# Kernel tuning notes

Measured on AMD Instinct MI355X. Metric: run time of the kernel, lower is better.

Reference implementation:

```python
import jax, jax.numpy as jnp
import numpy as np

NEG = -1e30

def setup_inputs() -> dict:
    key = jax.random.key(0)
    k1, k2, k3, k4, k5 = jax.random.split(key, 5)
    B, N, M, D = 32, 2048, 512, 512
    C = jax.random.normal(k1, (B, N, D), dtype=jnp.float32)
    Q = jax.random.normal(k2, (B, M, D), dtype=jnp.float32)
    Cmask = jax.random.randint(k3, (B, N), 0, 2, dtype=jnp.int32)
    Qmask = jax.random.randint(k4, (B, M), 0, 2, dtype=jnp.int32)
    # Linear(3*dim, 1, bias=False) weight, flattened to a (3*dim,) vector.
    bound = 1.0 / np.sqrt(3 * D)
    w = jax.random.uniform(k5, (3 * D,), dtype=jnp.float32, minval=-bound, maxval=bound)
    return {"C": C, "Q": Q, "Cmask": Cmask, "Qmask": Qmask, "w": w}

def reference(C, Q, Cmask, Qmask, w):
    D = C.shape[-1]
    w1, w2, w3 = w[:D], w[D:2 * D], w[2 * D:]
    # Trilinear similarity, decomposed: S = w1.Ct + w2.Qt + w3.(Ct*Qt)
    S = (jnp.einsum('bnd,d->bn', C, w1)[:, :, None]
         + jnp.einsum('bmd,d->bm', Q, w2)[:, None, :]
         + jnp.einsum('bnd,bmd->bnm', C * w3, Q))  # [B, N, M]
    Qm = Qmask.astype(S.dtype)[:, None, :]  # [B, 1, M]; 1 = masked
    Cm = Cmask.astype(S.dtype)[:, :, None]  # [B, N, 1]
    S1 = jax.nn.softmax(S * (1.0 - Qm) + Qm * NEG, axis=2)
    S2 = jax.nn.softmax(S * (1.0 - Cm) + Cm * NEG, axis=1)
    A = jnp.einsum('bnm,bmd->bnd', S1, Q)
    T = jnp.einsum('bnm,bnd->bmd', S2, C)     # S2^T @ C
    Bout = jnp.einsum('bnm,bmd->bnd', S1, T)  # S1 @ (S2^T @ C)
    return (A, Bout)
```

## Files before the change

kernel.cpp:

```cpp
#include <hip/hip_runtime.h>

#define BB 32
#define NN 2048
#define MM 512
#define DD 512
#define TS 64
#define KC 16
#define PAD 4
#define LDKH 40

typedef _Float16 half4f __attribute__((ext_vector_type(4)));
typedef _Float16 half8f __attribute__((ext_vector_type(8)));
typedef float    f32x16 __attribute__((ext_vector_type(16)));

__global__ __launch_bounds__(256) void k_dots(const float* __restrict__ C, const float* __restrict__ Q,
                                              const float* __restrict__ w,
                                              float* __restrict__ c1, float* __restrict__ q2) {
    int wid  = blockIdx.x * 4 + (threadIdx.x >> 6);
    int lane = threadIdx.x & 63;
    const int NR1 = BB * NN;
    const float* src; const float* wv; float* dst;
    if (wid < NR1) { src = C + (size_t)wid * DD; wv = w;       dst = c1 + wid; }
    else { int r = wid - NR1; src = Q + (size_t)r * DD; wv = w + DD; dst = q2 + r; }
    float4 a0 = *(const float4*)(src + lane * 8);
    float4 a1 = *(const float4*)(src + lane * 8 + 4);
    float4 b0 = *(const float4*)(wv  + lane * 8);
    float4 b1 = *(const float4*)(wv  + lane * 8 + 4);
    float s = a0.x * b0.x + a0.y * b0.y + a0.z * b0.z + a0.w * b0.w
            + a1.x * b1.x + a1.y * b1.y + a1.z * b1.z + a1.w * b1.w;
#pragma unroll
    for (int o = 32; o > 0; o >>= 1) s += __shfl_down(s, o);
    if (lane == 0) *dst = s;
}

__global__ __launch_bounds__(256) void k_qt(const float* __restrict__ Q, const int* __restrict__ Qmask,
                                            _Float16* __restrict__ Qt) {
    __shared__ float Ls[64][65];
    const int bid = blockIdx.x;
    const int b   = bid >> 6;
    const int rem = bid & 63;
    const int m0  = (rem >> 3) << 6;
    const int d0  = (rem & 7) << 6;
    const int tid = threadIdx.x;
    const int r   = tid >> 4;
    const int c4  = (tid & 15) << 2;
#pragma unroll
    for (int p = 0; p < 4; ++p) {
        float4 v = *(const float4*)(Q + ((size_t)(b * MM + m0 + r + p * 16)) * DD + d0 + c4);
        const int m = r + p * 16;
        Ls[c4 + 0][m] = v.x; Ls[c4 + 1][m] = v.y; Ls[c4 + 2][m] = v.z; Ls[c4 + 3][m] = v.w;
    }
    __syncthreads();
    float z[4];
#pragma unroll
    for (int i = 0; i < 4; ++i) z[i] = Qmask[b * MM + m0 + c4 + i] ? 0.f : 1.f;
#pragma unroll
    for (int p = 0; p < 4; ++p) {
        const int d = r + p * 16;
        half4f o;
#pragma unroll
        for (int i = 0; i < 4; ++i) o[i] = (_Float16)(Ls[d][c4 + i] * z[i]);
        *(half4f*)&Qt[((size_t)(b * DD + d0 + d)) * MM + m0 + c4] = o;
    }
}

__global__ __launch_bounds__(256) void k_ct(const float* __restrict__ C, _Float16* __restrict__ Ct) {
    __shared__ float Ls[64][65];
    const int bid = blockIdx.x;
    const int b   = bid >> 8;
    const int nn0 = ((bid >> 3) & 31) << 6;
    const int dd0 = (bid & 7) << 6;
    const int tid = threadIdx.x;
    const int r   = tid >> 4;
    const int c4  = (tid & 15) << 2;
#pragma unroll
    for (int p = 0; p < 4; ++p) {
        const int n = r + (p << 4);
        float4 v = *(const float4*)(C + ((size_t)(b * NN + nn0 + n)) * DD + dd0 + c4);
        Ls[c4 + 0][n] = v.x; Ls[c4 + 1][n] = v.y; Ls[c4 + 2][n] = v.z; Ls[c4 + 3][n] = v.w;
    }
    __syncthreads();
#pragma unroll
    for (int p = 0; p < 4; ++p) {
        const int d = r + (p << 4);
        half4f o;
#pragma unroll
        for (int i = 0; i < 4; ++i) o[i] = (_Float16)Ls[d][c4 + i];
        *(half4f*)&Ct[((size_t)(b * DD + dd0 + d)) * NN + nn0 + c4] = o;
    }
}

__global__ __launch_bounds__(256) void k_te(const _Float16* __restrict__ E, const int* __restrict__ Cmask,
                                            _Float16* __restrict__ Et) {
    __shared__ float Ls[64][65];
    const int bid = blockIdx.x;
    const int b   = bid >> 8;
    const int nn0 = ((bid >> 3) & 31) << 6;
    const int mm0 = (bid & 7) << 6;
    const int tid = threadIdx.x;
    const int r   = tid >> 4;
    const int c4  = (tid & 15) << 2;
#pragma unroll
    for (int p = 0; p < 4; ++p) {
        const int n = r + (p << 4);
        half4f v = *(const half4f*)&E[((size_t)(b * NN + nn0 + n)) * MM + mm0 + c4];
        const float z = Cmask[b * NN + nn0 + n] ? 0.f : 1.f;
        Ls[c4 + 0][n] = (float)v[0] * z; Ls[c4 + 1][n] = (float)v[1] * z;
        Ls[c4 + 2][n] = (float)v[2] * z; Ls[c4 + 3][n] = (float)v[3] * z;
    }
    __syncthreads();
#pragma unroll
    for (int p = 0; p < 4; ++p) {
        const int m = r + (p << 4);
        half4f o;
#pragma unroll
        for (int i = 0; i < 4; ++i) o[i] = (_Float16)Ls[m][c4 + i];
        *(half4f*)&Et[((size_t)(b * MM + mm0 + m)) * NN + nn0 + c4] = o;
    }
}

__global__ __launch_bounds__(256, 2) void k_sgemm(const float* __restrict__ C, const float* __restrict__ Q,
                                                  const float* __restrict__ w,
                                                  const int* __restrict__ Cmask, const int* __restrict__ Qmask,
                                                  const float* __restrict__ c1, const float* __restrict__ q2,
                                                  _Float16* __restrict__ E, float* __restrict__ rsum,
                                                  float* __restrict__ csum) {
    __shared__ _Float16 Ah[128 * LDKH], Al[128 * LDKH], Bh[128 * LDKH], Bl[128 * LDKH];
    __shared__ float rowp[128], colp[128], cmz[128], qmz[128], c1s[128], q2s[128];
    const int hw  = blockIdx.x;
    const int bid = ((hw & 7) << 8) | (hw >> 3);
    const int b   = bid >> 6;
    const int rem = bid & 63;
    const int n0  = (rem >> 2) << 7;
    const int m0  = (rem & 3) << 7;
    const int tid = threadIdx.x;
    const int lane = tid & 63;
    const int wid  = tid >> 6;
    const int wr = wid >> 1, wc = wid & 1;
    const int srow = tid >> 3;
    const int sc4  = (tid & 7) << 2;
    if (tid < 128) {
        rowp[tid] = 0.f; colp[tid] = 0.f;
        cmz[tid] = Cmask[b * NN + n0 + tid] ? 0.f : 1.f;
        c1s[tid] = c1[b * NN + n0 + tid];
    } else {
        const int t = tid - 128;
        qmz[t] = Qmask[b * MM + m0 + t] ? 0.f : 1.f;
        q2s[t] = q2[b * MM + m0 + t];
    }
    f32x16 accH[2][2] = {};
    f32x16 accX[2][2] = {};
    const int ar  = wr * 64 + (lane & 31);
    const int bc  = wc * 64 + (lane & 31);
    const int kof = (lane >> 5) << 3;
    const float* Cb = C + ((size_t)(b * NN + n0)) * DD;
    const float* Qb = Q + ((size_t)(b * MM + m0)) * DD;
    const float* w3 = w + 2 * DD;
    for (int k0 = 0; k0 < DD; k0 += 32) {
        float4 wv = *(const float4*)(w3 + k0 + sc4);
        float4 ca[4], qa[4];
#pragma unroll
        for (int p = 0; p < 4; ++p) {
            ca[p] = *(const float4*)(Cb + (size_t)(srow + (p << 5)) * DD + k0 + sc4);
            qa[p] = *(const float4*)(Qb + (size_t)(srow + (p << 5)) * DD + k0 + sc4);
        }
        __syncthreads();
#pragma unroll
        for (int p = 0; p < 4; ++p) {
            const int ofs = (srow + (p << 5)) * LDKH + sc4;
            float ax[4] = {ca[p].x * wv.x, ca[p].y * wv.y, ca[p].z * wv.z, ca[p].w * wv.w};
            float bx[4] = {qa[p].x, qa[p].y, qa[p].z, qa[p].w};
            half4f ah, al, bh, bl;
#pragma unroll
            for (int e = 0; e < 4; ++e) {
                _Float16 h = (_Float16)ax[e]; ah[e] = h;
                al[e] = (_Float16)((ax[e] - (float)h) * 2048.f);
                _Float16 g = (_Float16)bx[e]; bh[e] = g;
                bl[e] = (_Float16)((bx[e] - (float)g) * 2048.f);
            }
            *(half4f*)&Ah[ofs] = ah; *(half4f*)&Al[ofs] = al;
            *(half4f*)&Bh[ofs] = bh; *(half4f*)&Bl[ofs] = bl;
        }
        __syncthreads();
#pragma unroll
        for (int h = 0; h < 2; ++h) {
            const int ko = (h << 4) + kof;
            half8f ah0 = *(const half8f*)&Ah[ar * LDKH + ko];
            half8f ah1 = *(const half8f*)&Ah[(ar + 32) * LDKH + ko];
            half8f al0 = *(const half8f*)&Al[ar * LDKH + ko];
            half8f al1 = *(const half8f*)&Al[(ar + 32) * LDKH + ko];
            half8f bh0 = *(const half8f*)&Bh[bc * LDKH + ko];
            half8f bh1 = *(const half8f*)&Bh[(bc + 32) * LDKH + ko];
            half8f bl0 = *(const half8f*)&Bl[bc * LDKH + ko];
            half8f bl1 = *(const half8f*)&Bl[(bc + 32) * LDKH + ko];
            accH[0][0] = __builtin_amdgcn_mfma_f32_32x32x16_f16(ah0, bh0, accH[0][0], 0, 0, 0);
            accH[0][1] = __builtin_amdgcn_mfma_f32_32x32x16_f16(ah0, bh1, accH[0][1], 0, 0, 0);
            accH[1][0] = __builtin_amdgcn_mfma_f32_32x32x16_f16(ah1, bh0, accH[1][0], 0, 0, 0);
            accH[1][1] = __builtin_amdgcn_mfma_f32_32x32x16_f16(ah1, bh1, accH[1][1], 0, 0, 0);
            accX[0][0] = __builtin_amdgcn_mfma_f32_32x32x16_f16(ah0, bl0, accX[0][0], 0, 0, 0);
            accX[0][0] = __builtin_amdgcn_mfma_f32_32x32x16_f16(al0, bh0, accX[0][0], 0, 0, 0);
            accX[0][1] = __builtin_amdgcn_mfma_f32_32x32x16_f16(ah0, bl1, accX[0][1], 0, 0, 0);
            accX[0][1] = __builtin_amdgcn_mfma_f32_32x32x16_f16(al0, bh1, accX[0][1], 0, 0, 0);
            accX[1][0] = __builtin_amdgcn_mfma_f32_32x32x16_f16(ah1, bl0, accX[1][0], 0, 0, 0);
            accX[1][0] = __builtin_amdgcn_mfma_f32_32x32x16_f16(al1, bh0, accX[1][0], 0, 0, 0);
            accX[1][1] = __builtin_amdgcn_mfma_f32_32x32x16_f16(ah1, bl1, accX[1][1], 0, 0, 0);
            accX[1][1] = __builtin_amdgcn_mfma_f32_32x32x16_f16(al1, bh1, accX[1][1], 0, 0, 0);
        }
    }
    const float inv2k = 4.8828125e-4f;
    const int mcol0 = wc * 64 + (lane & 31);
    const float qz0 = qmz[mcol0], qz1 = qmz[mcol0 + 32];
    const float q2v0 = q2s[mcol0], q2v1 = q2s[mcol0 + 32];
    const int hi4 = (lane >> 5) << 2;
    float colacc0 = 0.f, colacc1 = 0.f;
#pragma unroll
    for (int i = 0; i < 2; ++i) {
#pragma unroll
        for (int r = 0; r < 16; ++r) {
            const int nloc = wr * 64 + i * 32 + (r & 3) + ((r >> 2) << 3) + hi4;
            const float base = c1s[nloc];
            float S0 = accH[i][0][r] + accX[i][0][r] * inv2k + base + q2v0;
            float S1 = accH[i][1][r] + accX[i][1][r] * inv2k + base + q2v1;
            float e0 = __expf(S0), e1 = __expf(S1);
            _Float16 h0 = (_Float16)e0, h1 = (_Float16)e1;
            float eq0 = (float)h0, eq1 = (float)h1;
            const size_t erow = ((size_t)(b * NN + n0 + nloc)) * MM + m0;
            E[erow + mcol0]      = h0;
            E[erow + mcol0 + 32] = h1;
            const float cz = cmz[nloc];
            colacc0 += eq0 * cz;
            colacc1 += eq1 * cz;
            float rv = eq0 * qz0 + eq1 * qz1;
            rv += __shfl_xor(rv, 1);  rv += __shfl_xor(rv, 2);
            rv += __shfl_xor(rv, 4);  rv += __shfl_xor(rv, 8);
            rv += __shfl_xor(rv, 16);
            if ((lane & 31) == 0) atomicAdd(&rowp[nloc], rv);
        }
    }
    atomicAdd(&colp[mcol0], colacc0);
    atomicAdd(&colp[mcol0 + 32], colacc1);
    __syncthreads();
    if (tid < 128) atomicAdd(&rsum[b * NN + n0 + tid], rowp[tid]);
    else atomicAdd(&csum[b * MM + m0 + tid - 128], colp[tid - 128]);
}

__global__ __launch_bounds__(256, 2) void k_T(const _Float16* __restrict__ Ct,
                                              const _Float16* __restrict__ Et,
                                              const float* __restrict__ csum,
                                              const int* __restrict__ Qmask,
                                              _Float16* __restrict__ Tt) {
    __shared__ _Float16 As[128 * LDKH];
    __shared__ _Float16 Bs[128 * LDKH];
    const int hw  = blockIdx.x;
    const int bid = ((hw & 7) << 6) | (hw >> 3);
    const int b   = bid >> 4;
    const int rem = bid & 15;
    const int d0  = (rem >> 2) << 7;
    const int m0  = (rem & 3) << 7;
    const int tid = threadIdx.x;
    const int lane = tid & 63;
    const int wid  = tid >> 6;
    const int wr = wid >> 1, wc = wid & 1;
    const int srow = tid >> 2;
    const int scol = (tid & 3) << 3;
    const _Float16* g0 = Ct + ((size_t)(b * DD + d0 + srow)) * NN + scol;
    const _Float16* g1 = Et + ((size_t)(b * MM + m0 + srow)) * NN + scol;
    const int wofs = srow * LDKH + scol;
    f32x16 acc[2][2] = {};
    const int ar  = wr * 64 + (lane & 31);
    const int bc  = wc * 64 + (lane & 31);
    const int kof = (lane >> 5) << 3;
    for (int k0 = 0; k0 < NN; k0 += 32) {
        half8f a0v = *(const half8f*)(g0 + k0);
        half8f a1v = *(const half8f*)(g0 + k0 + (size_t)64 * NN);
        half8f b0v = *(const half8f*)(g1 + k0);
        half8f b1v = *(const half8f*)(g1 + k0 + (size_t)64 * NN);
        __syncthreads();
        *(half8f*)&As[wofs]             = a0v;
        *(half8f*)&As[wofs + 64 * LDKH] = a1v;
        *(half8f*)&Bs[wofs]             = b0v;
        *(half8f*)&Bs[wofs + 64 * LDKH] = b1v;
        __syncthreads();
#pragma unroll
        for (int h = 0; h < 2; ++h) {
            const int ko = (h << 4) + kof;
            half8f a0 = *(const half8f*)&As[ar * LDKH + ko];
            half8f a1 = *(const half8f*)&As[(ar + 32) * LDKH + ko];
            half8f b0 = *(const half8f*)&Bs[bc * LDKH + ko];
            half8f b1 = *(const half8f*)&Bs[(bc + 32) * LDKH + ko];
            acc[0][0] = __builtin_amdgcn_mfma_f32_32x32x16_f16(a0, b0, acc[0][0], 0, 0, 0);
            acc[0][1] = __builtin_amdgcn_mfma_f32_32x32x16_f16(a0, b1, acc[0][1], 0, 0, 0);
            acc[1][0] = __builtin_amdgcn_mfma_f32_32x32x16_f16(a1, b0, acc[1][0], 0, 0, 0);
            acc[1][1] = __builtin_amdgcn_mfma_f32_32x32x16_f16(a1, b1, acc[1][1], 0, 0, 0);
        }
    }
    const int mc0 = m0 + wc * 64 + (lane & 31);
    const float s0 = (Qmask[b * MM + mc0]      ? 0.f : 1.f) / csum[b * MM + mc0];
    const float s1 = (Qmask[b * MM + mc0 + 32] ? 0.f : 1.f) / csum[b * MM + mc0 + 32];
    const int hi4 = (lane >> 5) << 2;
#pragma unroll
    for (int i = 0; i < 2; ++i) {
#pragma unroll
        for (int r = 0; r < 16; ++r) {
            const int d = d0 + wr * 64 + i * 32 + (r & 3) + ((r >> 2) << 3) + hi4;
            const size_t o = ((size_t)(b * DD + d)) * MM + mc0;
            Tt[o]      = (_Float16)(acc[i][0][r] * s0);
            Tt[o + 32] = (_Float16)(acc[i][1][r] * s1);
        }
    }
}

#define KS 32

__global__ __launch_bounds__(256, 2) void k_AB(const _Float16* __restrict__ E,
                                               const _Float16* __restrict__ Qt,
                                               const _Float16* __restrict__ Tt,
                                               const float* __restrict__ rsum,
                                               float* __restrict__ outA, float* __restrict__ outB) {
    __shared__ _Float16 Es[128 * LDKH];
    __shared__ _Float16 Ws[2][128 * LDKH];
    const int hw  = blockIdx.x;
    const int bid = ((hw & 7) << 8) | (hw >> 3);
    const int b   = bid >> 6;
    const int rem = bid & 63;
    const int n0  = (rem >> 2) << 7;
    const int d0  = (rem & 3) << 7;
    const int tid = threadIdx.x;
    const int lane = tid & 63;
    const int wid  = tid >> 6;
    const int wr = wid >> 1, wc = wid & 1;
    const int srow = tid >> 2;
    const int scol = (tid & 3) << 3;
    const _Float16* g0 = E  + ((size_t)(b * NN + n0 + srow)) * MM + scol;
    const _Float16* g1 = Qt + ((size_t)(b * DD + d0 + srow)) * MM + scol;
    const _Float16* g2 = Tt + ((size_t)(b * DD + d0 + srow)) * MM + scol;
    const int wofs = srow * LDKH + scol;
    f32x16 accA[2][2] = {};
    f32x16 accB[2][2] = {};
    const int ar  = wr * 64 + (lane & 31);
    const int bc  = wc * 64 + (lane & 31);
    const int kof = (lane >> 5) << 3;
    for (int k0 = 0; k0 < MM; k0 += KS) {
        half8f e0 = *(const half8f*)(g0 + k0);
        half8f e1 = *(const half8f*)(g0 + k0 + (size_t)64 * MM);
        half8f q0 = *(const half8f*)(g1 + k0);
        half8f q1 = *(const half8f*)(g1 + k0 + (size_t)64 * MM);
        half8f t0 = *(const half8f*)(g2 + k0);
        half8f t1 = *(const half8f*)(g2 + k0 + (size_t)64 * MM);
        __syncthreads();
        *(half8f*)&Es[wofs]                = e0;
        *(half8f*)&Es[wofs + 64 * LDKH]    = e1;
        *(half8f*)&Ws[0][wofs]             = q0;
        *(half8f*)&Ws[0][wofs + 64 * LDKH] = q1;
        *(half8f*)&Ws[1][wofs]             = t0;
        *(half8f*)&Ws[1][wofs + 64 * LDKH] = t1;
        __syncthreads();
#pragma unroll
        for (int h = 0; h < 2; ++h) {
            const int ko = (h << 4) + kof;
            half8f a0  = *(const half8f*)&Es[ar * LDKH + ko];
            half8f a1  = *(const half8f*)&Es[(ar + 32) * LDKH + ko];
            half8f bq0 = *(const half8f*)&Ws[0][bc * LDKH + ko];
            half8f bq1 = *(const half8f*)&Ws[0][(bc + 32) * LDKH + ko];
            half8f bt0 = *(const half8f*)&Ws[1][bc * LDKH + ko];
            half8f bt1 = *(const half8f*)&Ws[1][(bc + 32) * LDKH + ko];
            accA[0][0] = __builtin_amdgcn_mfma_f32_32x32x16_f16(a0, bq0, accA[0][0], 0, 0, 0);
            accA[0][1] = __builtin_amdgcn_mfma_f32_32x32x16_f16(a0, bq1, accA[0][1], 0, 0, 0);
            accA[1][0] = __builtin_amdgcn_mfma_f32_32x32x16_f16(a1, bq0, accA[1][0], 0, 0, 0);
            accA[1][1] = __builtin_amdgcn_mfma_f32_32x32x16_f16(a1, bq1, accA[1][1], 0, 0, 0);
            accB[0][0] = __builtin_amdgcn_mfma_f32_32x32x16_f16(a0, bt0, accB[0][0], 0, 0, 0);
            accB[0][1] = __builtin_amdgcn_mfma_f32_32x32x16_f16(a0, bt1, accB[0][1], 0, 0, 0);
            accB[1][0] = __builtin_amdgcn_mfma_f32_32x32x16_f16(a1, bt0, accB[1][0], 0, 0, 0);
            accB[1][1] = __builtin_amdgcn_mfma_f32_32x32x16_f16(a1, bt1, accB[1][1], 0, 0, 0);
        }
    }
    const int dc = d0 + wc * 64 + (lane & 31);
#pragma unroll
    for (int i = 0; i < 2; ++i) {
#pragma unroll
        for (int r = 0; r < 16; ++r) {
            const int row = (r & 3) + ((r >> 2) << 3) + ((lane >> 5) << 2);
            const int n = n0 + wr * 64 + i * 32 + row;
            const float inv = __builtin_amdgcn_rcpf(rsum[b * NN + n]);
            const size_t o = ((size_t)(b * NN + n)) * DD + dc;
            outA[o]      = accA[i][0][r] * inv;
            outA[o + 32] = accA[i][1][r] * inv;
            outB[o]      = accB[i][0][r] * inv;
            outB[o + 32] = accB[i][1][r] * inv;
        }
    }
}

extern "C" void kernel_launch(void* const* d_in, const int* in_sizes, int n_in,
                              void* d_out, int out_size, void* d_ws, size_t ws_size,
                              hipStream_t stream) {
    const float* C = (const float*)d_in[0];
    const float* Q = (const float*)d_in[1];
    const int* Cmask = (const int*)d_in[2];
    const int* Qmask = (const int*)d_in[3];
    const float* w  = (const float*)d_in[4];

    const size_t BNM = (size_t)BB * NN * MM;
    const size_t BMD = (size_t)BB * MM * DD;
    const size_t BND = (size_t)BB * NN * DD;
    const size_t BN  = (size_t)BB * NN;
    const size_t BM  = (size_t)BB * MM;

    _Float16* E  = (_Float16*)d_ws;
    _Float16* Tt = E + BNM;
    _Float16* Qt = Tt + BMD;
    float* fbase = (float*)(Qt + BMD);
    float* c1   = fbase;
    float* q2   = c1 + BN;
    float* rsum = q2 + BM;
    float* csum = rsum + BN;

    _Float16* Ct = (_Float16*)d_out;
    _Float16* Et = (_Float16*)((float*)d_out + BND);

    hipMemsetAsync(rsum, 0, (BN + BM) * sizeof(float), stream);

    k_dots<<<(int)((BN + BM) / 4), 256, 0, stream>>>(C, Q, w, c1, q2);
    k_qt<<<BB * 64, 256, 0, stream>>>(Q, Qmask, Qt);
    k_ct<<<BB * 256, 256, 0, stream>>>(C, Ct);
    k_sgemm<<<2048, 256, 0, stream>>>(C, Q, w, Cmask, Qmask, c1, q2, E, rsum, csum);
    k_te<<<BB * 256, 256, 0, stream>>>(E, Cmask, Et);
    k_T<<<512, 256, 0, stream>>>(Ct, Et, csum, Qmask, Tt);
    k_AB<<<2048, 256, 0, stream>>>(E, Qt, Tt, rsum,
                                   (float*)d_out, (float*)d_out + BND);
}
```

Before: 755.7 us.

## Pre-pack operands into MFMA fragment layout and stream GEMMs from global registers

```diff
diff --git a/kernel.cpp b/kernel.cpp
--- a/kernel.cpp
+++ b/kernel.cpp
@@ -4,128 +4,197 @@
 #define NN 2048
 #define MM 512
 #define DD 512
-#define TS 64
-#define KC 16
-#define PAD 4
-#define LDKH 40
-
-typedef _Float16 half4f __attribute__((ext_vector_type(4)));
+
 typedef _Float16 half8f __attribute__((ext_vector_type(8)));
 typedef float    f32x16 __attribute__((ext_vector_type(16)));
 
-__global__ __launch_bounds__(256) void k_dots(const float* __restrict__ C, const float* __restrict__ Q,
-                                              const float* __restrict__ w,
-                                              float* __restrict__ c1, float* __restrict__ q2) {
-    int wid  = blockIdx.x * 4 + (threadIdx.x >> 6);
-    int lane = threadIdx.x & 63;
-    const int NR1 = BB * NN;
-    const float* src; const float* wv; float* dst;
-    if (wid < NR1) { src = C + (size_t)wid * DD; wv = w;       dst = c1 + wid; }
-    else { int r = wid - NR1; src = Q + (size_t)r * DD; wv = w + DD; dst = q2 + r; }
-    float4 a0 = *(const float4*)(src + lane * 8);
-    float4 a1 = *(const float4*)(src + lane * 8 + 4);
-    float4 b0 = *(const float4*)(wv  + lane * 8);
-    float4 b1 = *(const float4*)(wv  + lane * 8 + 4);
-    float s = a0.x * b0.x + a0.y * b0.y + a0.z * b0.z + a0.w * b0.w
-            + a1.x * b1.x + a1.y * b1.y + a1.z * b1.z + a1.w * b1.w;
-#pragma unroll
-    for (int o = 32; o > 0; o >>= 1) s += __shfl_down(s, o);
-    if (lane == 0) *dst = s;
-}
-
-__global__ __launch_bounds__(256) void k_qt(const float* __restrict__ Q, const int* __restrict__ Qmask,
-                                            _Float16* __restrict__ Qt) {
-    __shared__ float Ls[64][65];
-    const int bid = blockIdx.x;
-    const int b   = bid >> 6;
-    const int rem = bid & 63;
-    const int m0  = (rem >> 3) << 6;
-    const int d0  = (rem & 7) << 6;
-    const int tid = threadIdx.x;
-    const int r   = tid >> 4;
-    const int c4  = (tid & 15) << 2;
-#pragma unroll
-    for (int p = 0; p < 4; ++p) {
-        float4 v = *(const float4*)(Q + ((size_t)(b * MM + m0 + r + p * 16)) * DD + d0 + c4);
-        const int m = r + p * 16;
-        Ls[c4 + 0][m] = v.x; Ls[c4 + 1][m] = v.y; Ls[c4 + 2][m] = v.z; Ls[c4 + 3][m] = v.w;
-    }
-    __syncthreads();
-    float z[4];
-#pragma unroll
-    for (int i = 0; i < 4; ++i) z[i] = Qmask[b * MM + m0 + c4 + i] ? 0.f : 1.f;
-#pragma unroll
-    for (int p = 0; p < 4; ++p) {
-        const int d = r + p * 16;
-        half4f o;
-#pragma unroll
-        for (int i = 0; i < 4; ++i) o[i] = (_Float16)(Ls[d][c4 + i] * z[i]);
-        *(half4f*)&Qt[((size_t)(b * DD + d0 + d)) * MM + m0 + c4] = o;
-    }
-}
-
-__global__ __launch_bounds__(256) void k_ct(const float* __restrict__ C, _Float16* __restrict__ Ct) {
+#define MFMA __builtin_amdgcn_mfma_f32_32x32x16_f16
+
+__device__ __forceinline__ int pidx(int r, int k, int K) {
+    return (r >> 7) * (K << 7) + ((k >> 4) << 11) + (((r >> 5) & 3) << 9)
+         + (((r & 31) + (((k >> 3) & 1) << 5)) << 3) + (k & 7);
+}
+__device__ __forceinline__ int kpart(int k) {
+    return ((k >> 4) << 11) + (((k >> 3) & 1) << 8) + (k & 7);
+}
+
+__global__ __launch_bounds__(256) void k_prepC(const float* __restrict__ C, const float* __restrict__ w,
+                                               float* __restrict__ c1, _Float16* __restrict__ PCt,
+                                               _Float16* __restrict__ PCh, _Float16* __restrict__ PCl) {
     __shared__ float Ls[64][65];
     const int bid = blockIdx.x;
     const int b   = bid >> 8;
     const int nn0 = ((bid >> 3) & 31) << 6;
     const int dd0 = (bid & 7) << 6;
     const int tid = threadIdx.x;
-    const int r   = tid >> 4;
-    const int c4  = (tid & 15) << 2;
+    const int nl  = tid >> 2;
+    const int dl  = (tid & 3) << 4;
+    const float* w1 = w;
+    const float* w3 = w + 2 * DD;
+    const size_t crow = ((size_t)(b * NN + nn0 + nl)) * DD + dd0 + dl;
+    float4 v[4], u[4], t[4];
 #pragma unroll
     for (int p = 0; p < 4; ++p) {
-        const int n = r + (p << 4);
-        float4 v = *(const float4*)(C + ((size_t)(b * NN + nn0 + n)) * DD + dd0 + c4);
-        Ls[c4 + 0][n] = v.x; Ls[c4 + 1][n] = v.y; Ls[c4 + 2][n] = v.z; Ls[c4 + 3][n] = v.w;
+        v[p] = *(const float4*)(C + crow + p * 4);
+        u[p] = *(const float4*)(w1 + dd0 + dl + p * 4);
+        t[p] = *(const float4*)(w3 + dd0 + dl + p * 4);
+    }
+    float s = 0.f;
+#pragma unroll
+    for (int p = 0; p < 4; ++p) s += v[p].x * u[p].x + v[p].y * u[p].y + v[p].z * u[p].z + v[p].w * u[p].w;
+    s += __shfl_xor(s, 1); s += __shfl_xor(s, 2);
+    if ((tid & 3) == 0) atomicAdd(&c1[b * NN + nn0 + nl], s);
+#pragma unroll
+    for (int p = 0; p < 4; ++p) {
+        Ls[dl + p * 4 + 0][nl] = v[p].x; Ls[dl + p * 4 + 1][nl] = v[p].y;
+        Ls[dl + p * 4 + 2][nl] = v[p].z; Ls[dl + p * 4 + 3][nl] = v[p].w;
+    }
+    const size_t pb = (size_t)b * NN * DD;
+#pragma unroll
+    for (int q = 0; q < 2; ++q) {
+        float x[8];
+#pragma unroll
+        for (int e = 0; e < 8; ++e) {
+            const int p = q * 2 + (e >> 2);
+            const float* vp = &v[p].x; const float* tp = &t[p].x;
+            x[e] = vp[e & 3] * tp[e & 3];
+        }
+        half8f hh, ll;
+#pragma unroll
+        for (int e = 0; e < 8; ++e) {
+            _Float16 h = (_Float16)x[e]; hh[e] = h;
+            ll[e] = (_Float16)((x[e] - (float)h) * 2048.f);
+        }
+        const int pi = pidx(nn0 + nl, dd0 + dl + q * 8, DD);
+        *(half8f*)&PCh[pb + pi] = hh;
+        *(half8f*)&PCl[pb + pi] = ll;
     }
     __syncthreads();
+    const int d2 = tid >> 2, n2 = (tid & 3) << 4;
+    const size_t tb = (size_t)b * DD * NN;
+#pragma unroll
+    for (int q = 0; q < 2; ++q) {
+        const int nc = n2 + q * 8;
+        half8f o;
+#pragma unroll
+        for (int j = 0; j < 8; ++j) o[j] = (_Float16)Ls[d2][nc + j];
+        *(half8f*)&PCt[tb + pidx(dd0 + d2, nn0 + nc, NN)] = o;
+    }
+}
+
+__global__ __launch_bounds__(256) void k_prepQ(const float* __restrict__ Q, const int* __restrict__ Qmask,
+                                               const float* __restrict__ w, float* __restrict__ q2,
+                                               _Float16* __restrict__ PQt,
+                                               _Float16* __restrict__ PQh, _Float16* __restrict__ PQl) {
+    __shared__ float Ls[64][65];
+    const int bid = blockIdx.x;
+    const int b   = bid >> 6;
+    const int rem = bid & 63;
+    const int mm0 = (rem >> 3) << 6;
+    const int dd0 = (rem & 7) << 6;
+    const int tid = threadIdx.x;
+    const int ml  = tid >> 2;
+    const int dl  = (tid & 3) << 4;
+    const float* w2 = w + DD;
+    const size_t qrow = ((size_t)(b * MM + mm0 + ml)) * DD + dd0 + dl;
+    float4 v[4], u[4];
 #pragma unroll
     for (int p = 0; p < 4; ++p) {
-        const int d = r + (p << 4);
-        half4f o;
-#pragma unroll
-        for (int i = 0; i < 4; ++i) o[i] = (_Float16)Ls[d][c4 + i];
-        *(half4f*)&Ct[((size_t)(b * DD + dd0 + d)) * NN + nn0 + c4] = o;
-    }
-}
-
-__global__ __launch_bounds__(256) void k_te(const _Float16* __restrict__ E, const int* __restrict__ Cmask,
-                                            _Float16* __restrict__ Et) {
+        v[p] = *(const float4*)(Q + qrow + p * 4);
+        u[p] = *(const float4*)(w2 + dd0 + dl + p * 4);
+    }
+    float s = 0.f;
+#pragma unroll
+    for (int p = 0; p < 4; ++p) s += v[p].x * u[p].x + v[p].y * u[p].y + v[p].z * u[p].z + v[p].w * u[p].w;
+    s += __shfl_xor(s, 1); s += __shfl_xor(s, 2);
+    if ((tid & 3) == 0) atomicAdd(&q2[b * MM + mm0 + ml], s);
+    const float z = Qmask[b * MM + mm0 + ml] ? 0.f : 1.f;
+#pragma unroll
+    for (int p = 0; p < 4; ++p) {
+        Ls[dl + p * 4 + 0][ml] = v[p].x * z; Ls[dl + p * 4 + 1][ml] = v[p].y * z;
+        Ls[dl + p * 4 + 2][ml] = v[p].z * z; Ls[dl + p * 4 + 3][ml] = v[p].w * z;
+    }
+    const size_t pb = (size_t)b * MM * DD;
+#pragma unroll
+    for (int q = 0; q < 2; ++q) {
+        float x[8];
+#pragma unroll
+        for (int e = 0; e < 8; ++e) {
+            const int p = q * 2 + (e >> 2);
+            const float* vp = &v[p].x;
+            x[e] = vp[e & 3];
+        }
+        half8f hh, ll;
+#pragma unroll
+        for (int e = 0; e < 8; ++e) {
+            _Float16 h = (_Float16)x[e]; hh[e] = h;
+            ll[e] = (_Float16)((x[e] - (float)h) * 2048.f);
+        }
+        const int pi = pidx(mm0 + ml, dd0 + dl + q * 8, DD);
+        *(half8f*)&PQh[pb + pi] = hh;
+        *(half8f*)&PQl[pb + pi] = ll;
+    }
+    __syncthreads();
+    const int d2 = tid >> 2, m2 = (tid & 3) << 4;
+    const size_t tb = (size_t)b * DD * MM;
+#pragma unroll
+    for (int q = 0; q < 2; ++q) {
+        const int mc = m2 + q * 8;
+        half8f o;
+#pragma unroll
+        for (int j = 0; j < 8; ++j) o[j] = (_Float16)Ls[d2][mc + j];
+        *(half8f*)&PQt[tb + pidx(dd0 + d2, mm0 + mc, MM)] = o;
+    }
+}
+
+__global__ __launch_bounds__(256) void k_te(const _Float16* __restrict__ PE, const int* __restrict__ Cmask,
+                                            _Float16* __restrict__ PEt) {
     __shared__ float Ls[64][65];
     const int bid = blockIdx.x;
     const int b   = bid >> 8;
     const int nn0 = ((bid >> 3) & 31) << 6;
     const int mm0 = (bid & 7) << 6;
     const int tid = threadIdx.x;
-    const int r   = tid >> 4;
-    const int c4  = (tid & 15) << 2;
-#pragma unroll
-    for (int p = 0; p < 4; ++p) {
-        const int n = r + (p << 4);
-        half4f v = *(const half4f*)&E[((size_t)(b * NN + nn0 + n)) * MM + mm0 + c4];
-        const float z = Cmask[b * NN + nn0 + n] ? 0.f : 1.f;
-        Ls[c4 + 0][n] = (float)v[0] * z; Ls[c4 + 1][n] = (float)v[1] * z;
-        Ls[c4 + 2][n] = (float)v[2] * z; Ls[c4 + 3][n] = (float)v[3] * z;
+    const int nl  = tid >> 2;
+    const int ml  = (tid & 3) << 4;
+    const float z = Cmask[b * NN + nn0 + nl] ? 0.f : 1.f;
+    const size_t eb = (size_t)b * NN * MM;
+#pragma unroll
+    for (int q = 0; q < 2; ++q) {
+        half8f v = *(const half8f*)&PE[eb + pidx(nn0 + nl, mm0 + ml + q * 8, MM)];
+#pragma unroll
+        for (int j = 0; j < 8; ++j) Ls[ml + q * 8 + j][nl] = (float)v[j] * z;
     }
     __syncthreads();
-#pragma unroll
-    for (int p = 0; p < 4; ++p) {
-        const int m = r + (p << 4);
-        half4f o;
-#pragma unroll
-        for (int i = 0; i < 4; ++i) o[i] = (_Float16)Ls[m][c4 + i];
-        *(half4f*)&Et[((size_t)(b * MM + mm0 + m)) * NN + nn0 + c4] = o;
-    }
-}
-
-__global__ __launch_bounds__(256, 2) void k_sgemm(const float* __restrict__ C, const float* __restrict__ Q,
-                                                  const float* __restrict__ w,
+    const int m2 = tid >> 2, n2 = (tid & 3) << 4;
+    const size_t tb = (size_t)b * MM * NN;
+#pragma unroll
+    for (int q = 0; q < 2; ++q) {
+        const int nc = n2 + q * 8;
+        half8f o;
+#pragma unroll
+        for (int j = 0; j < 8; ++j) o[j] = (_Float16)Ls[m2][nc + j];
+        *(half8f*)&PEt[tb + pidx(mm0 + m2, nn0 + nc, NN)] = o;
+    }
+}
+
+#define SG_LOAD(P, kc) { const int o_ = (kc) * 256;                                   \
+    P##ah0 = pAh[o_]; P##ah1 = pAh[o_ + 64]; P##al0 = pAl[o_]; P##al1 = pAl[o_ + 64]; \
+    P##bh0 = pBh[o_]; P##bh1 = pBh[o_ + 64]; P##bl0 = pBl[o_]; P##bl1 = pBl[o_ + 64]; }
+#define SG_STEP(A0,A1,L0,L1,B0,B1,D0,D1)                                     \
+    accH[0][0]=MFMA(A0,B0,accH[0][0],0,0,0); accH[0][1]=MFMA(A0,B1,accH[0][1],0,0,0); \
+    accH[1][0]=MFMA(A1,B0,accH[1][0],0,0,0); accH[1][1]=MFMA(A1,B1,accH[1][1],0,0,0); \
+    accX[0][0]=MFMA(A0,D0,accX[0][0],0,0,0); accX[0][0]=MFMA(L0,B0,accX[0][0],0,0,0); \
+    accX[0][1]=MFMA(A0,D1,accX[0][1],0,0,0); accX[0][1]=MFMA(L0,B1,accX[0][1],0,0,0); \
+    accX[1][0]=MFMA(A1,D0,accX[1][0],0,0,0); accX[1][0]=MFMA(L1,B0,accX[1][0],0,0,0); \
+    accX[1][1]=MFMA(A1,D1,accX[1][1],0,0,0); accX[1][1]=MFMA(L1,B1,accX[1][1],0,0,0);
+
+__global__ __launch_bounds__(256, 2) void k_sgemm(const _Float16* __restrict__ PCh, const _Float16* __restrict__ PCl,
+                                                  const _Float16* __restrict__ PQh, const _Float16* __restrict__ PQl,
                                                   const int* __restrict__ Cmask, const int* __restrict__ Qmask,
                                                   const float* __restrict__ c1, const float* __restrict__ q2,
                                                   _Float16* __restrict__ E, float* __restrict__ rsum,
                                                   float* __restrict__ csum) {
-    __shared__ _Float16 Ah[128 * LDKH], Al[128 * LDKH], Bh[128 * LDKH], Bl[128 * LDKH];
     __shared__ float rowp[128], colp[128], cmz[128], qmz[128], c1s[128], q2s[128];
     const int hw  = blockIdx.x;
     const int bid = ((hw & 7) << 8) | (hw >> 3);
@@ -137,8 +206,6 @@
     const int lane = tid & 63;
     const int wid  = tid >> 6;
     const int wr = wid >> 1, wc = wid & 1;
-    const int srow = tid >> 3;
-    const int sc4  = (tid & 7) << 2;
     if (tid < 128) {
         rowp[tid] = 0.f; colp[tid] = 0.f;
         cmz[tid] = Cmask[b * NN + n0 + tid] ? 0.f : 1.f;
@@ -148,70 +215,30 @@
         qmz[t] = Qmask[b * MM + m0 + t] ? 0.f : 1.f;
         q2s[t] = q2[b * MM + m0 + t];
     }
+    __syncthreads();
+    const half8f* pAh = (const half8f*)(PCh + (size_t)b * NN * DD + (size_t)n0 * DD) + wr * 128 + lane;
+    const half8f* pAl = (const half8f*)(PCl + (size_t)b * NN * DD + (size_t)n0 * DD) + wr * 128 + lane;
+    const half8f* pBh = (const half8f*)(PQh + (size_t)b * MM * DD + (size_t)m0 * DD) + wc * 128 + lane;
+    const half8f* pBl = (const half8f*)(PQl + (size_t)b * MM * DD + (size_t)m0 * DD) + wc * 128 + lane;
     f32x16 accH[2][2] = {};
     f32x16 accX[2][2] = {};
-    const int ar  = wr * 64 + (lane & 31);
-    const int bc  = wc * 64 + (lane & 31);
-    const int kof = (lane >> 5) << 3;
-    const float* Cb = C + ((size_t)(b * NN + n0)) * DD;
-    const float* Qb = Q + ((size_t)(b * MM + m0)) * DD;
-    const float* w3 = w + 2 * DD;
-    for (int k0 = 0; k0 < DD; k0 += 32) {
-        float4 wv = *(const float4*)(w3 + k0 + sc4);
-        float4 ca[4], qa[4];
-#pragma unroll
-        for (int p = 0; p < 4; ++p) {
-            ca[p] = *(const float4*)(Cb + (size_t)(srow + (p << 5)) * DD + k0 + sc4);
-            qa[p] = *(const float4*)(Qb + (size_t)(srow + (p << 5)) * DD + k0 + sc4);
-        }
-        __syncthreads();
-#pragma unroll
-        for (int p = 0; p < 4; ++p) {
-            const int ofs = (srow + (p << 5)) * LDKH + sc4;
-            float ax[4] = {ca[p].x * wv.x, ca[p].y * wv.y, ca[p].z * wv.z, ca[p].w * wv.w};
-            float bx[4] = {qa[p].x, qa[p].y, qa[p].z, qa[p].w};
-            half4f ah, al, bh, bl;
-#pragma unroll
-            for (int e = 0; e < 4; ++e) {
-                _Float16 h = (_Float16)ax[e]; ah[e] = h;
-                al[e] = (_Float16)((ax[e] - (float)h) * 2048.f);
-                _Float16 g = (_Float16)bx[e]; bh[e] = g;
-                bl[e] = (_Float16)((bx[e] - (float)g) * 2048.f);
-            }
-            *(half4f*)&Ah[ofs] = ah; *(half4f*)&Al[ofs] = al;
-            *(half4f*)&Bh[ofs] = bh; *(half4f*)&Bl[ofs] = bl;
-        }
-        __syncthreads();
-#pragma unroll
-        for (int h = 0; h < 2; ++h) {
-            const int ko = (h << 4) + kof;
-            half8f ah0 = *(const half8f*)&Ah[ar * LDKH + ko];
-            half8f ah1 = *(const half8f*)&Ah[(ar + 32) * LDKH + ko];
-            half8f al0 = *(const half8f*)&Al[ar * LDKH + ko];
-            half8f al1 = *(const half8f*)&Al[(ar + 32) * LDKH + ko];
-            half8f bh0 = *(const half8f*)&Bh[bc * LDKH + ko];
-            half8f bh1 = *(const half8f*)&Bh[(bc + 32) * LDKH + ko];
-            half8f bl0 = *(const half8f*)&Bl[bc * LDKH + ko];
-            half8f bl1 = *(const half8f*)&Bl[(bc + 32) * LDKH + ko];
-            accH[0][0] = __builtin_amdgcn_mfma_f32_32x32x16_f16(ah0, bh0, accH[0][0], 0, 0, 0);
-            accH[0][1] = __builtin_amdgcn_mfma_f32_32x32x16_f16(ah0, bh1, accH[0][1], 0, 0, 0);
-            accH[1][0] = __builtin_amdgcn_mfma_f32_32x32x16_f16(ah1, bh0, accH[1][0], 0, 0, 0);
-            accH[1][1] = __builtin_amdgcn_mfma_f32_32x32x16_f16(ah1, bh1, accH[1][1], 0, 0, 0);
-            accX[0][0] = __builtin_amdgcn_mfma_f32_32x32x16_f16(ah0, bl0, accX[0][0], 0, 0, 0);
-            accX[0][0] = __builtin_amdgcn_mfma_f32_32x32x16_f16(al0, bh0, accX[0][0], 0, 0, 0);
-            accX[0][1] = __builtin_amdgcn_mfma_f32_32x32x16_f16(ah0, bl1, accX[0][1], 0, 0, 0);
-            accX[0][1] = __builtin_amdgcn_mfma_f32_32x32x16_f16(al0, bh1, accX[0][1], 0, 0, 0);
-            accX[1][0] = __builtin_amdgcn_mfma_f32_32x32x16_f16(ah1, bl0, accX[1][0], 0, 0, 0);
-            accX[1][0] = __builtin_amdgcn_mfma_f32_32x32x16_f16(al1, bh0, accX[1][0], 0, 0, 0);
-            accX[1][1] = __builtin_amdgcn_mfma_f32_32x32x16_f16(ah1, bl1, accX[1][1], 0, 0, 0);
-            accX[1][1] = __builtin_amdgcn_mfma_f32_32x32x16_f16(al1, bh1, accX[1][1], 0, 0, 0);
-        }
+    half8f xah0, xah1, xal0, xal1, xbh0, xbh1, xbl0, xbl1;
+    half8f yah0, yah1, yal0, yal1, ybh0, ybh1, ybl0, ybl1;
+    SG_LOAD(x, 0);
+    for (int kc = 0; kc < 32; kc += 2) {
+        SG_LOAD(y, kc + 1);
+        SG_STEP(xah0, xah1, xal0, xal1, xbh0, xbh1, xbl0, xbl1);
+        if (kc + 2 < 32) SG_LOAD(x, kc + 2);
+        SG_STEP(yah0, yah1, yal0, yal1, ybh0, ybh1, ybl0, ybl1);
     }
     const float inv2k = 4.8828125e-4f;
     const int mcol0 = wc * 64 + (lane & 31);
     const float qz0 = qmz[mcol0], qz1 = qmz[mcol0 + 32];
     const float q2v0 = q2s[mcol0], q2v1 = q2s[mcol0 + 32];
     const int hi4 = (lane >> 5) << 2;
+    const size_t ebase = (size_t)b * NN * MM + (size_t)n0 * MM;
+    const int kp0 = kpart(m0 + mcol0);
+    const int kp1 = kpart(m0 + mcol0 + 32);
     float colacc0 = 0.f, colacc1 = 0.f;
 #pragma unroll
     for (int i = 0; i < 2; ++i) {
@@ -224,9 +251,9 @@
             float e0 = __expf(S0), e1 = __expf(S1);
             _Float16 h0 = (_Float16)e0, h1 = (_Float16)e1;
             float eq0 = (float)h0, eq1 = (float)h1;
-            const size_t erow = ((size_t)(b * NN + n0 + nloc)) * MM + m0;
-            E[erow + mcol0]      = h0;
-            E[erow + mcol0 + 32] = h1;
+            const int rp = (((nloc >> 5) & 3) << 9) + ((nloc & 31) << 3);
+            E[ebase + rp + kp0] = h0;
+            E[ebase + rp + kp1] = h1;
             const float cz = cmz[nloc];
             colacc0 += eq0 * cz;
             colacc1 += eq1 * cz;
@@ -244,13 +271,17 @@
     else atomicAdd(&csum[b * MM + m0 + tid - 128], colp[tid - 128]);
 }
 
-__global__ __launch_bounds__(256, 2) void k_T(const _Float16* __restrict__ Ct,
-                                              const _Float16* __restrict__ Et,
+#define KT_LOAD(P, kc) { const int o_ = (kc) * 256;                     \
+    P##a0 = pA[o_]; P##a1 = pA[o_ + 64]; P##b0 = pB[o_]; P##b1 = pB[o_ + 64]; }
+#define KT_STEP(A0,A1,B0,B1)                                            \
+    acc[0][0]=MFMA(A0,B0,acc[0][0],0,0,0); acc[0][1]=MFMA(A0,B1,acc[0][1],0,0,0); \
+    acc[1][0]=MFMA(A1,B0,acc[1][0],0,0,0); acc[1][1]=MFMA(A1,B1,acc[1][1],0,0,0);
+
+__global__ __launch_bounds__(256, 2) void k_T(const _Float16* __restrict__ PCt,
+                                              const _Float16* __restrict__ PEt,
                                               const float* __restrict__ csum,
                                               const int* __restrict__ Qmask,
                                               _Float16* __restrict__ Tt) {
-    __shared__ _Float16 As[128 * LDKH];
-    __shared__ _Float16 Bs[128 * LDKH];
     const int hw  = blockIdx.x;
     const int bid = ((hw & 7) << 6) | (hw >> 3);
     const int b   = bid >> 4;
@@ -261,64 +292,50 @@
     const int lane = tid & 63;
     const int wid  = tid >> 6;
     const int wr = wid >> 1, wc = wid & 1;
-    const int srow = tid >> 2;
-    const int scol = (tid & 3) << 3;
-    const _Float16* g0 = Ct + ((size_t)(b * DD + d0 + srow)) * NN + scol;
-    const _Float16* g1 = Et + ((size_t)(b * MM + m0 + srow)) * NN + scol;
-    const int wofs = srow * LDKH + scol;
+    const half8f* pA = (const half8f*)(PCt + (size_t)b * DD * NN + (size_t)d0 * NN) + wr * 128 + lane;
+    const half8f* pB = (const half8f*)(PEt + (size_t)b * MM * NN + (size_t)m0 * NN) + wc * 128 + lane;
     f32x16 acc[2][2] = {};
-    const int ar  = wr * 64 + (lane & 31);
-    const int bc  = wc * 64 + (lane & 31);
-    const int kof = (lane >> 5) << 3;
-    for (int k0 = 0; k0 < NN; k0 += 32) {
-        half8f a0v = *(const half8f*)(g0 + k0);
-        half8f a1v = *(const half8f*)(g0 + k0 + (size_t)64 * NN);
-        half8f b0v = *(const half8f*)(g1 + k0);
-        half8f b1v = *(const half8f*)(g1 + k0 + (size_t)64 * NN);
-        __syncthreads();
-        *(half8f*)&As[wofs]             = a0v;
-        *(half8f*)&As[wofs + 64 * LDKH] = a1v;
-        *(half8f*)&Bs[wofs]             = b0v;
-        *(half8f*)&Bs[wofs + 64 * LDKH] = b1v;
-        __syncthreads();
-#pragma unroll
-        for (int h = 0; h < 2; ++h) {
-            const int ko = (h << 4) + kof;
-            half8f a0 = *(const half8f*)&As[ar * LDKH + ko];
-            half8f a1 = *(const half8f*)&As[(ar + 32) * LDKH + ko];
-            half8f b0 = *(const half8f*)&Bs[bc * LDKH + ko];
-            half8f b1 = *(const half8f*)&Bs[(bc + 32) * LDKH + ko];
-            acc[0][0] = __builtin_amdgcn_mfma_f32_32x32x16_f16(a0, b0, acc[0][0], 0, 0, 0);
-            acc[0][1] = __builtin_amdgcn_mfma_f32_32x32x16_f16(a0, b1, acc[0][1], 0, 0, 0);
-            acc[1][0] = __builtin_amdgcn_mfma_f32_32x32x16_f16(a1, b0, acc[1][0], 0, 0, 0);
-            acc[1][1] = __builtin_amdgcn_mfma_f32_32x32x16_f16(a1, b1, acc[1][1], 0, 0, 0);
-        }
+    half8f xa0, xa1, xb0, xb1, ya0, ya1, yb0, yb1;
+    KT_LOAD(x, 0);
+    for (int kc = 0; kc < 128; kc += 2) {
+        KT_LOAD(y, kc + 1);
+        KT_STEP(xa0, xa1, xb0, xb1);
+        if (kc + 2 < 128) KT_LOAD(x, kc + 2);
+        KT_STEP(ya0, ya1, yb0, yb1);
     }
     const int mc0 = m0 + wc * 64 + (lane & 31);
     const float s0 = (Qmask[b * MM + mc0]      ? 0.f : 1.f) / csum[b * MM + mc0];
     const float s1 = (Qmask[b * MM + mc0 + 32] ? 0.f : 1.f) / csum[b * MM + mc0 + 32];
     const int hi4 = (lane >> 5) << 2;
+    const size_t tbase = (size_t)b * DD * MM + (size_t)d0 * MM;
+    const int kp0 = kpart(mc0);
+    const int kp1 = kpart(mc0 + 32);
 #pragma unroll
     for (int i = 0; i < 2; ++i) {
 #pragma unroll
         for (int r = 0; r < 16; ++r) {
-            const int d = d0 + wr * 64 + i * 32 + (r & 3) + ((r >> 2) << 3) + hi4;
-            const size_t o = ((size_t)(b * DD + d)) * MM + mc0;
-            Tt[o]      = (_Float16)(acc[i][0][r] * s0);
-            Tt[o + 32] = (_Float16)(acc[i][1][r] * s1);
-        }
-    }
-}
-
-#define KS 32
+            const int dloc = wr * 64 + i * 32 + (r & 3) + ((r >> 2) << 3) + hi4;
+            const int rp = (((dloc >> 5) & 3) << 9) + ((dloc & 31) << 3);
+            Tt[tbase + rp + kp0] = (_Float16)(acc[i][0][r] * s0);
+            Tt[tbase + rp + kp1] = (_Float16)(acc[i][1][r] * s1);
+        }
+    }
+}
+
+#define AB_LOAD(P, kc) { const int o_ = (kc) * 256;                     \
+    P##e0 = pE[o_]; P##e1 = pE[o_ + 64]; P##q0 = pQ[o_]; P##q1 = pQ[o_ + 64]; \
+    P##t0 = pT[o_]; P##t1 = pT[o_ + 64]; }
+#define AB_STEP(E0,E1,Q0,Q1,T0,T1)                                      \
+    accA[0][0]=MFMA(E0,Q0,accA[0][0],0,0,0); accA[0][1]=MFMA(E0,Q1,accA[0][1],0,0,0); \
+    accA[1][0]=MFMA(E1,Q0,accA[1][0],0,0,0); accA[1][1]=MFMA(E1,Q1,accA[1][1],0,0,0); \
+    accB[0][0]=MFMA(E0,T0,accB[0][0],0,0,0); accB[0][1]=MFMA(E0,T1,accB[0][1],0,0,0); \
+    accB[1][0]=MFMA(E1,T0,accB[1][0],0,0,0); accB[1][1]=MFMA(E1,T1,accB[1][1],0,0,0);
 
 __global__ __launch_bounds__(256, 2) void k_AB(const _Float16* __restrict__ E,
-                                               const _Float16* __restrict__ Qt,
+                                               const _Float16* __restrict__ PQt,
                                                const _Float16* __restrict__ Tt,
                                                const float* __restrict__ rsum,
                                                float* __restrict__ outA, float* __restrict__ outB) {
-    __shared__ _Float16 Es[128 * LDKH];
-    __shared__ _Float16 Ws[2][128 * LDKH];
     const int hw  = blockIdx.x;
     const int bid = ((hw & 7) << 8) | (hw >> 3);
     const int b   = bid >> 6;
@@ -329,50 +346,18 @@
     const int lane = tid & 63;
     const int wid  = tid >> 6;
     const int wr = wid >> 1, wc = wid & 1;
-    const int srow = tid >> 2;
-    const int scol = (tid & 3) << 3;
-    const _Float16* g0 = E  + ((size_t)(b * NN + n0 + srow)) * MM + scol;
-    const _Float16* g1 = Qt + ((size_t)(b * DD + d0 + srow)) * MM + scol;
-    const _Float16* g2 = Tt + ((size_t)(b * DD + d0 + srow)) * MM + scol;
-    const int wofs = srow * LDKH + scol;
+    const half8f* pE = (const half8f*)(E   + (size_t)b * NN * MM + (size_t)n0 * MM) + wr * 128 + lane;
+    const half8f* pQ = (const half8f*)(PQt + (size_t)b * DD * MM + (size_t)d0 * MM) + wc * 128 + lane;
+    const half8f* pT = (const half8f*)(Tt  + (size_t)b * DD * MM + (size_t)d0 * MM) + wc * 128 + lane;
     f32x16 accA[2][2] = {};
     f32x16 accB[2][2] = {};
-    const int ar  = wr * 64 + (lane & 31);
-    const int bc  = wc * 64 + (lane & 31);
-    const int kof = (lane >> 5) << 3;
-    for (int k0 = 0; k0 < MM; k0 += KS) {
-        half8f e0 = *(const half8f*)(g0 + k0);
-        half8f e1 = *(const half8f*)(g0 + k0 + (size_t)64 * MM);
-        half8f q0 = *(const half8f*)(g1 + k0);
-        half8f q1 = *(const half8f*)(g1 + k0 + (size_t)64 * MM);
-        half8f t0 = *(const half8f*)(g2 + k0);
-        half8f t1 = *(const half8f*)(g2 + k0 + (size_t)64 * MM);
-        __syncthreads();
-        *(half8f*)&Es[wofs]                = e0;
-        *(half8f*)&Es[wofs + 64 * LDKH]    = e1;
-        *(half8f*)&Ws[0][wofs]             = q0;
-        *(half8f*)&Ws[0][wofs + 64 * LDKH] = q1;
-        *(half8f*)&Ws[1][wofs]             = t0;
-        *(half8f*)&Ws[1][wofs + 64 * LDKH] = t1;
-        __syncthreads();
-#pragma unroll
-        for (int h = 0; h < 2; ++h) {
-            const int ko = (h << 4) + kof;
-            half8f a0  = *(const half8f*)&Es[ar * LDKH + ko];
-            half8f a1  = *(const half8f*)&Es[(ar + 32) * LDKH + ko];
-            half8f bq0 = *(const half8f*)&Ws[0][bc * LDKH + ko];
-            half8f bq1 = *(const half8f*)&Ws[0][(bc + 32) * LDKH + ko];
-            half8f bt0 = *(const half8f*)&Ws[1][bc * LDKH + ko];
-            half8f bt1 = *(const half8f*)&Ws[1][(bc + 32) * LDKH + ko];
-            accA[0][0] = __builtin_amdgcn_mfma_f32_32x32x16_f16(a0, bq0, accA[0][0], 0, 0, 0);
-            accA[0][1] = __builtin_amdgcn_mfma_f32_32x32x16_f16(a0, bq1, accA[0][1], 0, 0, 0);
-            accA[1][0] = __builtin_amdgcn_mfma_f32_32x32x16_f16(a1, bq0, accA[1][0], 0, 0, 0);
-            accA[1][1] = __builtin_amdgcn_mfma_f32_32x32x16_f16(a1, bq1, accA[1][1], 0, 0, 0);
-            accB[0][0] = __builtin_amdgcn_mfma_f32_32x32x16_f16(a0, bt0, accB[0][0], 0, 0, 0);
-            accB[0][1] = __builtin_amdgcn_mfma_f32_32x32x16_f16(a0, bt1, accB[0][1], 0, 0, 0);
-            accB[1][0] = __builtin_amdgcn_mfma_f32_32x32x16_f16(a1, bt0, accB[1][0], 0, 0, 0);
-            accB[1][1] = __builtin_amdgcn_mfma_f32_32x32x16_f16(a1, bt1, accB[1][1], 0, 0, 0);
-        }
+    half8f xe0, xe1, xq0, xq1, xt0, xt1, ye0, ye1, yq0, yq1, yt0, yt1;
+    AB_LOAD(x, 0);
+    for (int kc = 0; kc < 32; kc += 2) {
+        AB_LOAD(y, kc + 1);
+        AB_STEP(xe0, xe1, xq0, xq1, xt0, xt1);
+        if (kc + 2 < 32) AB_LOAD(x, kc + 2);
+        AB_STEP(ye0, ye1, yq0, yq1, yt0, yt1);
     }
     const int dc = d0 + wc * 64 + (lane & 31);
 #pragma unroll
@@ -406,26 +391,28 @@
     const size_t BN  = (size_t)BB * NN;
     const size_t BM  = (size_t)BB * MM;
 
-    _Float16* E  = (_Float16*)d_ws;
-    _Float16* Tt = E + BNM;
-    _Float16* Qt = Tt + BMD;
-    float* fbase = (float*)(Qt + BMD);
-    float* c1   = fbase;
+    _Float16* E   = (_Float16*)d_ws;
+    _Float16* Tt  = E + BNM;
+    _Float16* PQt = Tt + BMD;
+    float* c1   = (float*)(PQt + BMD);
     float* q2   = c1 + BN;
     float* rsum = q2 + BM;
     float* csum = rsum + BN;
 
-    _Float16* Ct = (_Float16*)d_out;
-    _Float16* Et = (_Float16*)((float*)d_out + BND);
-
-    hipMemsetAsync(rsum, 0, (BN + BM) * sizeof(float), stream);
-
-    k_dots<<<(int)((BN + BM) / 4), 256, 0, stream>>>(C, Q, w, c1, q2);
-    k_qt<<<BB * 64, 256, 0, stream>>>(Q, Qmask, Qt);
-    k_ct<<<BB * 256, 256, 0, stream>>>(C, Ct);
-    k_sgemm<<<2048, 256, 0, stream>>>(C, Q, w, Cmask, Qmask, c1, q2, E, rsum, csum);
-    k_te<<<BB * 256, 256, 0, stream>>>(E, Cmask, Et);
-    k_T<<<512, 256, 0, stream>>>(Ct, Et, csum, Qmask, Tt);
-    k_AB<<<2048, 256, 0, stream>>>(E, Qt, Tt, rsum,
+    _Float16* PCt = (_Float16*)d_out;
+    _Float16* PCh = PCt + BND;
+    _Float16* PCl = PCh + BND;
+    _Float16* PQh = PCl + BND;
+    _Float16* PQl = PQh + BMD;
+    _Float16* PEt = PCh;
+
+    hipMemsetAsync(c1, 0, 2 * (BN + BM) * sizeof(float), stream);
+
+    k_prepQ<<<BB * 64, 256, 0, stream>>>(Q, Qmask, w, q2, PQt, PQh, PQl);
+    k_prepC<<<BB * 256, 256, 0, stream>>>(C, w, c1, PCt, PCh, PCl);
+    k_sgemm<<<2048, 256, 0, stream>>>(PCh, PCl, PQh, PQl, Cmask, Qmask, c1, q2, E, rsum, csum);
+    k_te<<<BB * 256, 256, 0, stream>>>(E, Cmask, PEt);
+    k_T<<<512, 256, 0, stream>>>(PCt, PEt, csum, Qmask, Tt);
+    k_AB<<<2048, 256, 0, stream>>>(E, PQt, Tt, rsum,
                                    (float*)d_out, (float*)d_out + BND);
 }
```

Measured after the change: 880.8 us. 1.17x slower.
